# Performance work log

Measured on AMD Instinct MI355X. Metric: run time of the kernel, lower is better.

## Reference

```python
import jax, jax.numpy as jnp
import numpy as np

D_MODEL = 512
D_INNER = 1024      # expand * d_model
NHEADS = 16         # d_inner // headdim, headdim = d_model // num_heads = 64
HEADDIM = 64
DSTATE = 64
DCONV = 4           # window_size
DFF = 2048
B, LM, LT = 16, 1024, 512


def _rmsnorm(x, eps=1e-6):
    return x * jax.lax.rsqrt(jnp.mean(x * x, axis=-1, keepdims=True) + eps)


def setup_inputs():
    key = jax.random.key(0)
    ks = jax.random.split(key, 10)
    conv_dim = D_INNER + 2 * DSTATE
    d_in_proj = 2 * D_INNER + 2 * DSTATE + NHEADS
    return {
        'tgt': jax.random.normal(ks[0], (B, LT, D_MODEL), jnp.float32),
        'memory': jax.random.normal(ks[1], (B, LM, D_MODEL), jnp.float32),
        'mem_mask': jnp.ones((B, LM), jnp.float32),
        'tgt_mask': jnp.ones((B, LT), jnp.float32),
        'in_proj_w': jax.random.normal(ks[2], (d_in_proj, D_MODEL), jnp.float32) * 0.02,
        'conv_w': jax.random.normal(ks[3], (conv_dim, DCONV), jnp.float32) * 0.2,
        'conv_b': jnp.zeros((conv_dim,), jnp.float32),
        'dt_bias': jax.random.uniform(ks[4], (NHEADS,), jnp.float32, -4.0, -2.0),
        'A_log': jnp.log(jax.random.uniform(ks[5], (NHEADS,), jnp.float32, 1.0, 16.0)),
        'D': jnp.ones((NHEADS,), jnp.float32),
        'norm_w': jnp.ones((D_INNER,), jnp.float32),
        'out_proj_w': jax.random.normal(ks[6], (D_MODEL, D_INNER), jnp.float32) * 0.02,
        'fc1_w': jax.random.normal(ks[7], (DFF, D_MODEL), jnp.float32) * 0.02,
        'fc1_b': jnp.zeros((DFF,), jnp.float32),
        'fc2_w': jax.random.normal(ks[8], (D_MODEL, DFF), jnp.float32) * 0.02,
        'fc2_b': jnp.zeros((D_MODEL,), jnp.float32),
    }


def _mamba2(u, in_proj_w, conv_w, conv_b, dt_bias, A_log, D, norm_w, out_proj_w):
    # u: (B, L, d_model) -- Mamba2-style selective scan (causal, ngroups=1)
    b, L, _ = u.shape
    zxbcdt = jnp.einsum('bld,ed->ble', u, in_proj_w)  # (B,L,2192)
    z = zxbcdt[..., :D_INNER]
    xBC = zxbcdt[..., D_INNER:D_INNER + D_INNER + 2 * DSTATE]
    dt = zxbcdt[..., -NHEADS:]

    # causal depthwise conv1d, kernel = DCONV, then swish
    xBC_pad = jnp.pad(xBC, ((0, 0), (DCONV - 1, 0), (0, 0)))
    conv = conv_b
    conv = sum(conv_w[:, k] * xBC_pad[:, k:k + L] for k in range(DCONV)) + conv_b
    xBC = jax.nn.silu(conv)

    x = xBC[..., :D_INNER].reshape(b, L, NHEADS, HEADDIM)   # (B,L,H,P)
    Bm = xBC[..., D_INNER:D_INNER + DSTATE]                  # (B,L,N)
    Cm = xBC[..., D_INNER + DSTATE:]                         # (B,L,N)

    dt = jax.nn.softplus(dt + dt_bias)                       # (B,L,H)
    A = -jnp.exp(A_log)                                      # (H,)
    a = jnp.exp(dt * A)                                      # (B,L,H) decay

    def step(h, inputs):
        a_t, dt_t, x_t, B_t, C_t = inputs
        # h: (B,H,P,N)
        h = a_t[:, :, None, None] * h + (dt_t[:, :, None] * x_t)[..., None] * B_t[:, None, None, :]
        y = jnp.einsum('bhpn,bn->bhp', h, C_t)
        return h, y

    h0 = jnp.zeros((b, NHEADS, HEADDIM, DSTATE), u.dtype)
    xs = (jnp.moveaxis(a, 1, 0), jnp.moveaxis(dt, 1, 0), jnp.moveaxis(x, 1, 0),
          jnp.moveaxis(Bm, 1, 0), jnp.moveaxis(Cm, 1, 0))
    _, ys = jax.lax.scan(step, h0, xs)                       # (L,B,H,P)
    y = jnp.moveaxis(ys, 0, 1) + D[None, None, :, None] * x  # skip term
    y = y.reshape(b, L, D_INNER)

    # gated RMSNorm + out_proj
    y = y * jax.nn.silu(z)
    y = _rmsnorm(y, 1e-5) * norm_w
    return jnp.einsum('ble,de->bld', y, out_proj_w)


def _forward(tgt, memory, mem_mask, tgt_mask, in_proj_w, conv_w, conv_b, dt_bias,
             A_log, D, norm_w, out_proj_w, fc1_w, fc1_b, fc2_w, fc2_b):
    tgt = tgt * tgt_mask[..., None]
    tgt1 = _rmsnorm(tgt)
    memory = memory * mem_mask[..., None]
    u = jnp.concatenate([memory, tgt1], axis=1)
    mask = jnp.concatenate([mem_mask, tgt_mask], axis=1)
    u = u * mask[..., None]
    tgt2 = _mamba2(u, in_proj_w, conv_w, conv_b, dt_bias, A_log, D, norm_w, out_proj_w)
    tgt2 = tgt2[:, -tgt1.shape[1]:]
    tgt = tgt + tgt2  # dropout = identity (eval)
    tgt1 = _rmsnorm(tgt)
    h = jax.nn.gelu(jnp.einsum('bld,fd->blf', tgt1, fc1_w) + fc1_b, approximate=False)
    tgt2 = jnp.einsum('blf,df->bld', h, fc2_w) + fc2_b
    return tgt + tgt2


def reference(tgt, memory, mem_mask, tgt_mask, in_proj_w, conv_w, conv_b, dt_bias,
              A_log, D, norm_w, out_proj_w, fc1_w, fc1_b, fc2_w, fc2_b):
    return _forward(tgt, memory, mem_mask, tgt_mask, in_proj_w, conv_w, conv_b, dt_bias,
                    A_log, D, norm_w, out_proj_w, fc1_w, fc1_b, fc2_w, fc2_b)
```

## Files before the change

### kernel.cpp

```cpp
#include <hip/hip_runtime.h>
#include <cstddef>

#define BB 16
#define LMM 1024
#define LTT 512
#define LL 1536
#define DMODEL 512
#define DINNER 1024
#define NH 16
#define DIPROJ 2192
#define DFF2 2048

typedef __bf16 bf16_t;
typedef bf16_t bf16x2 __attribute__((ext_vector_type(2)));
typedef bf16_t bf16x4 __attribute__((ext_vector_type(4)));
typedef bf16_t bf16x8 __attribute__((ext_vector_type(8)));
typedef float f32x4 __attribute__((ext_vector_type(4)));

typedef __attribute__((address_space(3))) void lds_void;
typedef const __attribute__((address_space(1))) void glb_void;

__device__ __forceinline__ void gload16(const void* g, void* l) {
  __builtin_amdgcn_global_load_lds((glb_void*)g, (lds_void*)l, 16, 0, 0);
}

__device__ inline float block_sum(float v, float* sbuf) {
#pragma unroll
  for (int off = 32; off > 0; off >>= 1) v += __shfl_xor(v, off, 64);
  int w = threadIdx.x >> 6;
  if ((threadIdx.x & 63) == 0) sbuf[w] = v;
  __syncthreads();
  return sbuf[0] + sbuf[1] + sbuf[2] + sbuf[3];
}

__global__ __launch_bounds__(256)
void cvt_all(const float* __restrict__ s0, const float* __restrict__ s1,
             const float* __restrict__ s2, const float* __restrict__ s3,
             bf16_t* __restrict__ dst)
{
  int i = (blockIdx.x * 256 + threadIdx.x) * 4;
  if (i >= 3743744) return;
  const float* src;
  int off;
  if (i < 1122304)      { src = s0; off = i; }
  else if (i < 1646592) { src = s1; off = i - 1122304; }
  else if (i < 2695168) { src = s2; off = i - 1646592; }
  else                  { src = s3; off = i - 2695168; }
  float4 v = *(const float4*)&src[off];
  bf16x4 o;
  o[0] = (bf16_t)v.x; o[1] = (bf16_t)v.y; o[2] = (bf16_t)v.z; o[3] = (bf16_t)v.w;
  *(bf16x4*)&dst[i] = o;
}

__global__ __launch_bounds__(256)
void prep_u(const float* __restrict__ tgt, const float* __restrict__ memory,
            const float* __restrict__ mem_mask, const float* __restrict__ tgt_mask,
            bf16_t* __restrict__ u, float* __restrict__ tgtm)
{
  __shared__ float sbuf[4];
  const int row = blockIdx.x;
  const int b = row / LL;
  const int t = row - b * LL;
  const int tid = threadIdx.x;
  if (t < LMM) {
    float m = mem_mask[b * LMM + t];
    float s = m * m;
    const float* src = memory + ((size_t)b * LMM + t) * DMODEL;
    float2 v = *(const float2*)&src[tid * 2];
    bf16x2 o; o[0] = (bf16_t)(v.x * s); o[1] = (bf16_t)(v.y * s);
    *(bf16x2*)&u[(size_t)row * DMODEL + tid * 2] = o;
  } else {
    const int tt = t - LMM;
    float mk = tgt_mask[b * LTT + tt];
    const float* src = tgt + ((size_t)b * LTT + tt) * DMODEL;
    float2 v = *(const float2*)&src[tid * 2];
    v.x *= mk; v.y *= mk;
    *(float2*)&tgtm[((size_t)b * LTT + tt) * DMODEL + tid * 2] = v;
    float ss = block_sum(v.x * v.x + v.y * v.y, sbuf);
    float inv = rsqrtf(ss * (1.0f / 512.0f) + 1e-6f) * mk;
    bf16x2 o; o[0] = (bf16_t)(v.x * inv); o[1] = (bf16_t)(v.y * inv);
    *(bf16x2*)&u[(size_t)row * DMODEL + tid * 2] = o;
  }
}

template<int EPI>
__global__ __launch_bounds__(256)
void gemm_abf(const bf16_t* __restrict__ A, const bf16_t* __restrict__ W,
              int M, int N, int K,
              float* __restrict__ Cf, const float* __restrict__ bias,
              const float* __restrict__ res)
{
  const int nbx = gridDim.x;
  const int nwg = nbx * gridDim.y;
  int flat = blockIdx.y * nbx + blockIdx.x;
  int swz = (flat & 7) * (nwg >> 3) + (flat >> 3);
  const int m0 = (swz / nbx) * 128;
  const int n0 = (swz % nbx) * 128;
  __shared__ __align__(16) bf16_t As[128 * 64];
  __shared__ __align__(16) bf16_t Bs[128 * 64];
  const int tid = threadIdx.x;
  const int lane = tid & 63;
  const int wid = tid >> 6;
  const int wr = (wid >> 1) * 64, wc = (wid & 1) * 64;
  const int r = lane & 15;
  const int g = lane >> 4;
  const int r7 = r & 7;
  const int lrow = lane >> 3;
  const int sslot = (lane & 7) ^ lrow;

  int arow[4], brow[4];
#pragma unroll
  for (int ci = 0; ci < 4; ++ci) {
    int tr = wid * 32 + ci * 8 + lrow;
    arow[ci] = m0 + tr;
    int bn = n0 + tr;
    brow[ci] = bn < N ? bn : N - 1;
  }

  f32x4 acc[4][4];
#pragma unroll
  for (int m = 0; m < 4; ++m)
#pragma unroll
    for (int n = 0; n < 4; ++n) acc[m][n] = (f32x4){0.f, 0.f, 0.f, 0.f};

  for (int kt = 0; kt < K; kt += 64) {
#pragma unroll
    for (int ci = 0; ci < 4; ++ci) {
      int chunk = wid * 4 + ci;
      gload16(A + (size_t)arow[ci] * K + kt + sslot * 8, &As[chunk * 512]);
      gload16(W + (size_t)brow[ci] * K + kt + sslot * 8, &Bs[chunk * 512]);
    }
    __syncthreads();
#pragma unroll
    for (int c = 0; c < 2; ++c) {
      bf16x8 af[4], bfr[4];
#pragma unroll
      for (int m = 0; m < 4; ++m) {
        int row = wr + m * 16 + r;
        af[m] = *(const bf16x8*)&As[row * 64 + (((c * 4 + g) ^ r7) * 8)];
      }
#pragma unroll
      for (int n = 0; n < 4; ++n) {
        int row = wc + n * 16 + r;
        bfr[n] = *(const bf16x8*)&Bs[row * 64 + (((c * 4 + g) ^ r7) * 8)];
      }
#pragma unroll
      for (int m = 0; m < 4; ++m)
#pragma unroll
        for (int n = 0; n < 4; ++n)
          acc[m][n] = __builtin_amdgcn_mfma_f32_16x16x32_bf16(af[m], bfr[n], acc[m][n], 0, 0, 0);
    }
    __syncthreads();
  }

#pragma unroll
  for (int m = 0; m < 4; ++m) {
#pragma unroll
    for (int n = 0; n < 4; ++n) {
      int gcol = n0 + wc + n * 16 + r;
      if (gcol >= N) continue;
#pragma unroll
      for (int j = 0; j < 4; ++j) {
        float v = acc[m][n][j];
        int grow = m0 + wr + m * 16 + g * 4 + j;
        if (EPI == 2) v += bias[gcol] + res[(size_t)grow * N + gcol];
        else          v += res[(size_t)grow * N + gcol];
        Cf[(size_t)grow * N + gcol] = v;
      }
    }
  }
}

template<int EPI>
__global__ __launch_bounds__(512)
void gemm_big(const bf16_t* __restrict__ A, const bf16_t* __restrict__ W,
              int M, int N, int K,
              bf16_t* __restrict__ Cb, const float* __restrict__ bias,
              bf16_t* __restrict__ zbuf, bf16_t* __restrict__ xbc,
              float* __restrict__ dts, float* __restrict__ labuf,
              const float* __restrict__ dt_bias, const float* __restrict__ A_log)
{
  const int nbx = gridDim.x;
  const int nwg = nbx * gridDim.y;
  int flat = blockIdx.y * nbx + blockIdx.x;
  int swz = (flat & 7) * (nwg >> 3) + (flat >> 3);
  const int m0 = (swz / nbx) * 256;
  const int n0 = (swz % nbx) * 128;
  int bq = 0, tbase = 0;
  if (EPI == 4) {
    bq = m0 / LL; tbase = m0 - bq * LL;
    if (n0 + 128 <= DINNER && tbase + 256 <= LMM) return;
  }
  __shared__ __align__(16) bf16_t As[256 * 64];
  __shared__ __align__(16) bf16_t Bs[128 * 64];
  const int tid = threadIdx.x;
  const int lane = tid & 63;
  const int wid = tid >> 6;
  const int wr = (wid >> 1) * 64;
  const int wc = (wid & 1) * 64;
  const int r = lane & 15;
  const int g = lane >> 4;
  const int r7 = r & 7;
  const int lrow = lane >> 3;
  const int sslot = (lane & 7) ^ lrow;

  int arow[4], brow[2];
#pragma unroll
  for (int ci = 0; ci < 4; ++ci) arow[ci] = m0 + wid * 32 + ci * 8 + lrow;
#pragma unroll
  for (int ci = 0; ci < 2; ++ci) {
    int bn = n0 + wid * 16 + ci * 8 + lrow;
    brow[ci] = bn < N ? bn : N - 1;
  }

  f32x4 acc[4][4];
#pragma unroll
  for (int m = 0; m < 4; ++m)
#pragma unroll
    for (int n = 0; n < 4; ++n) acc[m][n] = (f32x4){0.f, 0.f, 0.f, 0.f};

  for (int kt = 0; kt < K; kt += 64) {
#pragma unroll
    for (int ci = 0; ci < 4; ++ci)
      gload16(A + (size_t)arow[ci] * K + kt + sslot * 8, &As[(wid * 4 + ci) * 512]);
#pragma unroll
    for (int ci = 0; ci < 2; ++ci)
      gload16(W + (size_t)brow[ci] * K + kt + sslot * 8, &Bs[(wid * 2 + ci) * 512]);
    __syncthreads();
#pragma unroll
    for (int c = 0; c < 2; ++c) {
      bf16x8 af[4], bfr[4];
#pragma unroll
      for (int m = 0; m < 4; ++m) {
        int row = wr + m * 16 + r;
        af[m] = *(const bf16x8*)&As[row * 64 + (((c * 4 + g) ^ r7) * 8)];
      }
#pragma unroll
      for (int n = 0; n < 4; ++n) {
        int row = wc + n * 16 + r;
        bfr[n] = *(const bf16x8*)&Bs[row * 64 + (((c * 4 + g) ^ r7) * 8)];
      }
#pragma unroll
      for (int m = 0; m < 4; ++m)
#pragma unroll
        for (int n = 0; n < 4; ++n)
          acc[m][n] = __builtin_amdgcn_mfma_f32_16x16x32_bf16(af[m], bfr[n], acc[m][n], 0, 0, 0);
    }
    __syncthreads();
  }

#pragma unroll
  for (int m = 0; m < 4; ++m) {
#pragma unroll
    for (int n = 0; n < 4; ++n) {
      int gcol = n0 + wc + n * 16 + r;
      if (gcol >= N) continue;
#pragma unroll
      for (int j = 0; j < 4; ++j) {
        float v = acc[m][n][j];
        int lrow2 = wr + m * 16 + g * 4 + j;
        if (EPI == 4) {
          int t = tbase + lrow2;
          if (gcol < DINNER) {
            if (t >= LMM)
              zbuf[(((size_t)(bq * LTT + t - LMM)) << 10) + gcol] = (bf16_t)v;
          } else if (gcol < DINNER + 1152) {
            xbc[(size_t)(bq * LL + t) * 1152 + (gcol - DINNER)] = (bf16_t)v;
          } else {
            int h = gcol - 2176;
            float raw = v + dt_bias[h];
            float d = raw > 20.f ? raw : log1pf(expf(raw));
            size_t ix = (size_t)(bq * LL + t) * 16 + h;
            dts[ix] = d;
            labuf[ix] = -expf(A_log[h]) * d;
          }
        } else {
          int grow = m0 + lrow2;
          v += bias[gcol];
          v = 0.5f * v * (1.f + erff(v * 0.70710678f));
          Cb[(size_t)grow * N + gcol] = (bf16_t)v;
        }
      }
    }
  }
}

__global__ __launch_bounds__(256)
void sbc_k(const bf16_t* __restrict__ xbc, const float* __restrict__ cw,
           const float* __restrict__ cb, bf16_t* __restrict__ BtG,
           bf16_t* __restrict__ Sg, bf16_t* __restrict__ CcG)
{
  __shared__ __align__(16) bf16_t rawBC[132 * 128];
  __shared__ __align__(16) bf16_t CB[128 * 128];
  __shared__ float wls[128 * 4];
  __shared__ float bls[128];
  const int c = blockIdx.x, b = blockIdx.y;
  const int t0 = c * 128;
  const int tid = threadIdx.x, lane = tid & 63, wid = tid >> 6;
  const int r = lane & 15, g = lane >> 4;

  if (tid < 128) {
    int gch = 1024 + tid;
#pragma unroll
    for (int k = 0; k < 4; ++k) wls[tid * 4 + k] = cw[gch * 4 + k];
    bls[tid] = cb[gch];
  }
#pragma unroll
  for (int ci = 0; ci < 9; ++ci) {
    int chunk = ci * 4 + wid;
    if (chunk < 33) {
      int F = chunk * 1024 + lane * 16;
      int row = F >> 8, off = F & 255;
      gload16(xbc + (size_t)(b * LL + t0 - 3 + row) * 1152 + 1024 + off / 2,
              &rawBC[chunk * 512]);
    }
  }
  __syncthreads();
  if (c == 0 && tid < 48) {
    bf16x8 z;
#pragma unroll
    for (int j = 0; j < 8; ++j) z[j] = (bf16_t)0.f;
    *(bf16x8*)&rawBC[tid * 8] = z;
  }
  __syncthreads();
#pragma unroll 2
  for (int it = 0; it < 64; ++it) {
    int o = tid + it * 256;
    int t = o >> 7, ch = o & 127;
    float a0 = bls[ch];
#pragma unroll
    for (int kk = 0; kk < 4; ++kk)
      a0 = fmaf(wls[ch * 4 + kk], (float)rawBC[(t + kk) * 128 + ch], a0);
    float sv = a0 / (1.f + expf(-a0));
    int slot = ch >> 3;
    int swslot = (slot & 8) | ((slot & 7) ^ (t & 7));
    CB[t * 128 + swslot * 8 + (ch & 7)] = (bf16_t)sv;
    if (c >= 8 && ch >= 64) {
      int n = ch - 64;
      CcG[(((size_t)(b * 4 + (c - 8)) * 128 + t)) * 64 + (((n >> 3) ^ (t & 7)) << 3) + (n & 7)] = (bf16_t)sv;
    }
  }
  __syncthreads();
  {
    int n = tid & 63, tb = tid >> 6;
#pragma unroll
    for (int s8 = 0; s8 < 4; ++s8) {
      int ts = tb * 32 + s8 * 8;
      bf16x8 v;
#pragma unroll
      for (int e = 0; e < 8; ++e) {
        int t = ts + e;
        int slot = (n >> 3) ^ (t & 7);
        v[e] = CB[t * 128 + slot * 8 + (n & 7)];
      }
      *(bf16x8*)&BtG[((size_t)(b * 12 + c) * 64 + n) * 128 + ((((ts >> 3) ^ (n & 7))) << 3)] = v;
    }
  }
  if (c >= 8) {
    f32x4 sacc[2][8];
#pragma unroll
    for (int tt = 0; tt < 2; ++tt)
#pragma unroll
      for (int ct = 0; ct < 8; ++ct) sacc[tt][ct] = (f32x4){0.f, 0.f, 0.f, 0.f};
    const int ctn = 2 * wid + 2;
#pragma unroll
    for (int kk = 0; kk < 2; ++kk) {
      bf16x8 ca[2];
#pragma unroll
      for (int tt = 0; tt < 2; ++tt) {
        int trow = wid * 32 + tt * 16 + r;
        int slot = (64 + kk * 32 + g * 8) >> 3;
        int sw = (slot & 8) | ((slot & 7) ^ (trow & 7));
        ca[tt] = *(const bf16x8*)&CB[trow * 128 + sw * 8];
      }
#pragma unroll
      for (int ct = 0; ct < 8; ++ct) {
        if (ct < ctn) {
          int taur = ct * 16 + r;
          int sw = ((kk * 4 + g) ^ (taur & 7));
          bf16x8 bb = *(const bf16x8*)&CB[taur * 128 + sw * 8];
          sacc[0][ct] = __builtin_amdgcn_mfma_f32_16x16x32_bf16(ca[0], bb, sacc[0][ct], 0, 0, 0);
          sacc[1][ct] = __builtin_amdgcn_mfma_f32_16x16x32_bf16(ca[1], bb, sacc[1][ct], 0, 0, 0);
        }
      }
    }
    size_t sbase = (size_t)(b * 4 + (c - 8)) * 16384;
#pragma unroll
    for (int tt = 0; tt < 2; ++tt)
#pragma unroll
      for (int ct = 0; ct < 8; ++ct) {
        if (ct < ctn) {
#pragma unroll
          for (int j = 0; j < 4; ++j) {
            int ta = wid * 32 + tt * 16 + g * 4 + j;
            int tau = ct * 16 + r;
            Sg[sbase + ta * 128 + (tau ^ ((ta & 7) << 3))] = (bf16_t)sacc[tt][ct][j];
          }
        }
      }
  }
}

__global__ __launch_bounds__(256)
void ssd_hend(const bf16_t* __restrict__ xbc, const float* __restrict__ dts,
              const float* __restrict__ labuf, const float* __restrict__ cw,
              const float* __restrict__ cb, const bf16_t* __restrict__ BtG,
              bf16_t* __restrict__ hend, float* __restrict__ Lacum,
              float* __restrict__ Ak)
{
  __shared__ __align__(16) bf16_t rawX[136 * 64];
  __shared__ __align__(16) bf16_t Xt[64 * 128];
  __shared__ __align__(16) bf16_t Bt[64 * 128];
  __shared__ float wv[128];
  __shared__ float wls[64 * 4];
  __shared__ float bls[64];
  const int c = blockIdx.x;
  const int bh = blockIdx.y;
  const int b = bh >> 4, h = bh & 15;
  const int t0 = c * 128;
  const int tid = threadIdx.x, lane = tid & 63, wid = tid >> 6;
  const int r = lane & 15, g = lane >> 4;

  if (tid < 64) {
    int gch = h * 64 + tid;
#pragma unroll
    for (int k = 0; k < 4; ++k) wls[tid * 4 + k] = cw[gch * 4 + k];
    bls[tid] = cb[gch];
  }
#pragma unroll
  for (int ci = 0; ci < 5; ++ci) {
    int chunk = ci * 4 + wid;
    if (chunk < 17) {
      int F = chunk * 1024 + lane * 16;
      int row = F >> 7, off = F & 127;
      gload16(xbc + (size_t)(b * LL + t0 - 3 + row) * 1152 + h * 64 + off / 2,
              &rawX[chunk * 512]);
    }
  }
#pragma unroll
  for (int ci = 0; ci < 4; ++ci) {
    int chunk = ci * 4 + wid;
    int F = chunk * 1024 + lane * 16;
    gload16(BtG + (size_t)(b * 12 + c) * 8192 + F / 2, &Bt[chunk * 512]);
  }
  __syncthreads();
  if (c == 0 && tid < 24) {
    bf16x8 z;
#pragma unroll
    for (int j = 0; j < 8; ++j) z[j] = (bf16_t)0.f;
    *(bf16x8*)&rawX[tid * 8] = z;
  }
  if (tid < 64) {
    float v0 = labuf[(size_t)(b * LL + t0 + tid) * 16 + h];
    float v1 = labuf[(size_t)(b * LL + t0 + 64 + tid) * 16 + h];
    float d0 = dts[(size_t)(b * LL + t0 + tid) * 16 + h];
    float d1 = dts[(size_t)(b * LL + t0 + 64 + tid) * 16 + h];
#pragma unroll
    for (int d = 1; d < 64; d <<= 1) { float t_ = __shfl(v0, tid - d, 64); if (tid >= d) v0 += t_; }
    float T0 = __shfl(v0, 63, 64);
#pragma unroll
    for (int d = 1; d < 64; d <<= 1) { float t_ = __shfl(v1, tid - d, 64); if (tid >= d) v1 += t_; }
    v1 += T0;
    float Ls = __shfl(v1, 63, 64);
    wv[tid] = expf(Ls - v0) * d0; wv[64 + tid] = expf(Ls - v1) * d1;
    Lacum[(size_t)(bh * 12 + c) * 128 + tid] = v0;
    Lacum[(size_t)(bh * 12 + c) * 128 + 64 + tid] = v1;
    if (tid == 0) Ak[bh * 12 + c] = expf(Ls);
  }
  __syncthreads();
  {
    int p = tid & 63, tb = (tid >> 6) * 32;
    float w0 = wls[p * 4], w1 = wls[p * 4 + 1], w2 = wls[p * 4 + 2], w3 = wls[p * 4 + 3];
    float bb0 = bls[p];
    int sw = (p & 7) << 3;
#pragma unroll
    for (int i8 = 0; i8 < 4; ++i8) {
      bf16x8 ov;
#pragma unroll
      for (int e = 0; e < 8; ++e) {
        int t = tb + i8 * 8 + e;
        float a0 = bb0;
        a0 = fmaf(w0, (float)rawX[(t + 0) * 64 + p], a0);
        a0 = fmaf(w1, (float)rawX[(t + 1) * 64 + p], a0);
        a0 = fmaf(w2, (float)rawX[(t + 2) * 64 + p], a0);
        a0 = fmaf(w3, (float)rawX[(t + 3) * 64 + p], a0);
        ov[e] = (bf16_t)(a0 / (1.f + expf(-a0)));
      }
      *(bf16x8*)&Xt[p * 128 + ((tb + i8 * 8) ^ sw)] = ov;
    }
  }
  __syncthreads();
  f32x4 acc[4];
#pragma unroll
  for (int n = 0; n < 4; ++n) acc[n] = (f32x4){0.f, 0.f, 0.f, 0.f};
  const int prow = wid * 16 + r;
#pragma unroll
  for (int kk = 0; kk < 4; ++kk) {
    int k0 = kk * 32 + g * 8;
    bf16x8 xv = *(const bf16x8*)&Xt[prow * 128 + (k0 ^ ((prow & 7) << 3))];
    bf16x8 af;
#pragma unroll
    for (int j = 0; j < 8; ++j) af[j] = (bf16_t)((float)xv[j] * wv[k0 + j]);
#pragma unroll
    for (int nt = 0; nt < 4; ++nt) {
      int nrow = nt * 16 + r;
      bf16x8 bf_ = *(const bf16x8*)&Bt[nrow * 128 + (k0 ^ ((nrow & 7) << 3))];
      acc[nt] = __builtin_amdgcn_mfma_f32_16x16x32_bf16(af, bf_, acc[nt], 0, 0, 0);
    }
  }
  size_t base = ((size_t)(bh * 12 + c)) * 4096;
#pragma unroll
  for (int nt = 0; nt < 4; ++nt)
#pragma unroll
    for (int j = 0; j < 4; ++j)
      hend[base + (size_t)(wid * 16 + g * 4 + j) * 64 + nt * 16 + r] = (bf16_t)acc[nt][j];
}

__global__ __launch_bounds__(256)
void ssd_y(const bf16_t* __restrict__ xbc, const float* __restrict__ dts,
           const bf16_t* __restrict__ hend, const float* __restrict__ Ak,
           const float* __restrict__ Lacum, const bf16_t* __restrict__ Sg,
           const bf16_t* __restrict__ CcG, const float* __restrict__ cw,
           const float* __restrict__ cb, const float* __restrict__ Dp,
           bf16_t* __restrict__ ybuf)
{
  __shared__ __align__(16) char region0[32768];
  __shared__ __align__(16) bf16_t Xt[64 * 128];
  __shared__ __align__(16) bf16_t Cs[128 * 64];
  __shared__ __align__(16) bf16_t hts[64 * 64];
  __shared__ float Lat[128];
  __shared__ float dtv[128];
  __shared__ float wls[64 * 4];
  __shared__ float bls[64];
  bf16_t* rawX = (bf16_t*)region0;
  bf16_t* Gs   = (bf16_t*)region0;
  const int c = 8 + blockIdx.x;
  const int bh = blockIdx.y;
  const int b = bh >> 4, h = bh & 15;
  const int t0 = c * 128;
  const int tid = threadIdx.x, lane = tid & 63, wid = tid >> 6;
  const int r = lane & 15, g = lane >> 4;

  if (tid < 64) {
    int gch = h * 64 + tid;
#pragma unroll
    for (int k = 0; k < 4; ++k) wls[tid * 4 + k] = cw[gch * 4 + k];
    bls[tid] = cb[gch];
  }
  if (tid < 128) {
    Lat[tid] = Lacum[(size_t)(bh * 12 + c) * 128 + tid];
    dtv[tid] = dts[(size_t)(b * LL + t0 + tid) * 16 + h];
  }
#pragma unroll
  for (int ci = 0; ci < 5; ++ci) {
    int chunk = ci * 4 + wid;
    if (chunk < 17) {
      int F = chunk * 1024 + lane * 16;
      int row = F >> 7, off = F & 127;
      gload16(xbc + (size_t)(b * LL + t0 - 3 + row) * 1152 + h * 64 + off / 2,
              &rawX[chunk * 512]);
    }
  }
#pragma unroll
  for (int ci = 0; ci < 4; ++ci) {
    int chunk = ci * 4 + wid;
    int F = chunk * 1024 + lane * 16;
    gload16(CcG + (size_t)(b * 4 + (c - 8)) * 8192 + F / 2, &Cs[chunk * 512]);
  }
  {
    float hin[16];
#pragma unroll
    for (int e = 0; e < 16; ++e) hin[e] = 0.f;
    float accp = 1.f;
    for (int k = c - 1; k >= 0; --k) {
      const bf16_t* hp = hend + ((size_t)(bh * 12 + k)) * 4096 + tid * 16;
      bf16x8 e0 = *(const bf16x8*)hp;
      bf16x8 e1 = *(const bf16x8*)(hp + 8);
#pragma unroll
      for (int j = 0; j < 8; ++j) {
        hin[j]     = fmaf(accp, (float)e0[j], hin[j]);
        hin[j + 8] = fmaf(accp, (float)e1[j], hin[j + 8]);
      }
      accp *= Ak[bh * 12 + k];
    }
    int p = tid >> 2, n0 = (tid & 3) * 16;
    bf16x8 o0, o1;
#pragma unroll
    for (int j = 0; j < 8; ++j) { o0[j] = (bf16_t)hin[j]; o1[j] = (bf16_t)hin[j + 8]; }
    int p7 = p & 7;
    *(bf16x8*)&hts[p * 64 + (((n0 >> 3) ^ p7) << 3)] = o0;
    *(bf16x8*)&hts[p * 64 + ((((n0 >> 3) + 1) ^ p7) << 3)] = o1;
  }
  __syncthreads();
  {
    int p = tid & 63, tb = (tid >> 6) * 32;
    float w0 = wls[p * 4], w1 = wls[p * 4 + 1], w2 = wls[p * 4 + 2], w3 = wls[p * 4 + 3];
    float bb0 = bls[p];
    int sw = (p & 7) << 3;
#pragma unroll
    for (int i8 = 0; i8 < 4; ++i8) {
      bf16x8 ov;
#pragma unroll
      for (int e = 0; e < 8; ++e) {
        int t = tb + i8 * 8 + e;
        float a0 = bb0;
        a0 = fmaf(w0, (float)rawX[(t + 0) * 64 + p], a0);
        a0 = fmaf(w1, (float)rawX[(t + 1) * 64 + p], a0);
        a0 = fmaf(w2, (float)rawX[(t + 2) * 64 + p], a0);
        a0 = fmaf(w3, (float)rawX[(t + 3) * 64 + p], a0);
        ov[e] = (bf16_t)(a0 / (1.f + expf(-a0)));
      }
      *(bf16x8*)&Xt[p * 128 + ((tb + i8 * 8) ^ sw)] = ov;
    }
  }
  __syncthreads();
  {
    size_t sbase = (size_t)(b * 4 + (c - 8)) * 16384;
#pragma unroll
    for (int it = 0; it < 8; ++it) {
      int o = tid + it * 256;
      int ta = o >> 4, sl = o & 15;
      bf16x8 sv = *(const bf16x8*)&Sg[sbase + ta * 128 + sl * 8];
      int tau0 = (sl ^ (ta & 7)) * 8;
      float Lta = Lat[ta];
      bf16x8 gv;
#pragma unroll
      for (int e = 0; e < 8; ++e) {
        int tau = tau0 + e;
        float xa = (tau <= ta) ? (Lta - Lat[tau]) : -1e30f;
        gv[e] = (bf16_t)(expf(xa) * dtv[tau] * (float)sv[e]);
      }
      *(bf16x8*)&Gs[ta * 128 + sl * 8] = gv;
    }
  }
  __syncthreads();

  bf16x8 caf[2][2];
#pragma unroll
  for (int tt = 0; tt < 2; ++tt)
#pragma unroll
    for (int kk = 0; kk < 2; ++kk) {
      int trow = wid * 32 + tt * 16 + r;
      caf[tt][kk] = *(const bf16x8*)&Cs[trow * 64 + ((((kk * 4 + g)) ^ (trow & 7)) << 3)];
    }

  f32x4 accY[2][4], acc2[2][4];
#pragma unroll
  for (int tt = 0; tt < 2; ++tt)
#pragma unroll
    for (int pt = 0; pt < 4; ++pt) {
      accY[tt][pt] = (f32x4){0.f, 0.f, 0.f, 0.f};
      acc2[tt][pt] = (f32x4){0.f, 0.f, 0.f, 0.f};
    }
#pragma unroll
  for (int tt = 0; tt < 2; ++tt) {
    int trow = wid * 32 + tt * 16 + r;
#pragma unroll
    for (int kk = 0; kk < 4; ++kk) {
      if (kk <= wid) {
        int k0 = kk * 32 + g * 8;
        bf16x8 ga = *(const bf16x8*)&Gs[trow * 128 + (k0 ^ ((trow & 7) << 3))];
#pragma unroll
        for (int pt = 0; pt < 4; ++pt) {
          int prow = pt * 16 + r;
          bf16x8 xb = *(const bf16x8*)&Xt[prow * 128 + (k0 ^ ((prow & 7) << 3))];
          accY[tt][pt] = __builtin_amdgcn_mfma_f32_16x16x32_bf16(ga, xb, accY[tt][pt], 0, 0, 0);
        }
      }
    }
#pragma unroll
    for (int kk = 0; kk < 2; ++kk) {
#pragma unroll
      for (int pt = 0; pt < 4; ++pt) {
        int prow = pt * 16 + r;
        bf16x8 hb = *(const bf16x8*)&hts[prow * 64 + ((((kk * 4 + g)) ^ (prow & 7)) << 3)];
        acc2[tt][pt] = __builtin_amdgcn_mfma_f32_16x16x32_bf16(caf[tt][kk], hb, acc2[tt][pt], 0, 0, 0);
      }
    }
  }

  const float Dh = Dp[h];
#pragma unroll
  for (int tt = 0; tt < 2; ++tt) {
#pragma unroll
    for (int j = 0; j < 4; ++j) {
      int trow = wid * 32 + tt * 16 + g * 4 + j;
      float el = expf(Lat[trow]);
      size_t yrow = ((size_t)(b * LTT + (c - 8) * 128 + trow)) << 10;
#pragma unroll
      for (int pt = 0; pt < 4; ++pt) {
        int p = pt * 16 + r;
        float xv = (float)Xt[p * 128 + (trow ^ ((p & 7) << 3))];
        float yv = accY[tt][pt][j] + el * acc2[tt][pt][j] + Dh * xv;
        ybuf[yrow + h * 64 + p] = (bf16_t)yv;
      }
    }
  }
}

__global__ __launch_bounds__(256)
void gate_norm_k(const bf16_t* __restrict__ zbuf, const bf16_t* __restrict__ ybuf,
                 const float* __restrict__ norm_w, bf16_t* __restrict__ yn)
{
  __shared__ float sbuf[4];
  const int row = blockIdx.x;
  const int tid = threadIdx.x;
  bf16x4 yv = *(const bf16x4*)&ybuf[(size_t)row * DINNER + tid * 4];
  bf16x4 zv = *(const bf16x4*)&zbuf[(size_t)row * DINNER + tid * 4];
  float v[4];
#pragma unroll
  for (int c = 0; c < 4; ++c) {
    float y = (float)yv[c], z = (float)zv[c];
    v[c] = y * (z / (1.f + expf(-z)));
  }
  float ss = block_sum(v[0]*v[0] + v[1]*v[1] + v[2]*v[2] + v[3]*v[3], sbuf);
  float inv = rsqrtf(ss * (1.f / 1024.f) + 1e-5f);
  float4 nw = *(const float4*)&norm_w[tid * 4];
  bf16x4 o;
  o[0] = (bf16_t)(v[0] * inv * nw.x); o[1] = (bf16_t)(v[1] * inv * nw.y);
  o[2] = (bf16_t)(v[2] * inv * nw.z); o[3] = (bf16_t)(v[3] * inv * nw.w);
  *(bf16x4*)&yn[(size_t)row * DINNER + tid * 4] = o;
}

__global__ __launch_bounds__(256)
void rms_k(const float* __restrict__ in, bf16_t* __restrict__ out)
{
  __shared__ float sbuf[4];
  const int row = blockIdx.x;
  const int tid = threadIdx.x;
  float2 v = *(const float2*)&in[(size_t)row * DMODEL + tid * 2];
  float ss = block_sum(v.x * v.x + v.y * v.y, sbuf);
  float inv = rsqrtf(ss * (1.f / 512.f) + 1e-6f);
  bf16x2 o; o[0] = (bf16_t)(v.x * inv); o[1] = (bf16_t)(v.y * inv);
  *(bf16x2*)&out[(size_t)row * DMODEL + tid * 2] = o;
}

extern "C" void kernel_launch(void* const* d_in, const int* in_sizes, int n_in,
                              void* d_out, int out_size, void* d_ws, size_t ws_size,
                              hipStream_t stream)
{
  const float* tgt        = (const float*)d_in[0];
  const float* memory     = (const float*)d_in[1];
  const float* mem_mask   = (const float*)d_in[2];
  const float* tgt_mask   = (const float*)d_in[3];
  const float* in_proj_w  = (const float*)d_in[4];
  const float* conv_w     = (const float*)d_in[5];
  const float* conv_b     = (const float*)d_in[6];
  const float* dt_bias    = (const float*)d_in[7];
  const float* A_log      = (const float*)d_in[8];
  const float* Dp         = (const float*)d_in[9];
  const float* norm_w     = (const float*)d_in[10];
  const float* out_proj_w = (const float*)d_in[11];
  const float* fc1_w      = (const float*)d_in[12];
  const float* fc1_b      = (const float*)d_in[13];
  const float* fc2_w      = (const float*)d_in[14];
  const float* fc2_b      = (const float*)d_in[15];

  char* wsb = (char*)d_ws;
  bf16_t* u     = (bf16_t*)(wsb + 0);
  bf16_t* zbuf  = (bf16_t*)(wsb + 25165824);
  bf16_t* xbc   = (bf16_t*)(wsb + 41943040);
  float*  dts   = (float*)(wsb + 98566144);
  float*  labuf = (float*)(wsb + 100139008);
  float*  tgtm  = (float*)(wsb + 101711872);
  bf16_t* hend  = (bf16_t*)(wsb + 118489088);
  float*  Lacum = (float*)(wsb + 143667200);
  float*  Akb   = (float*)(wsb + 145240064);
  bf16_t* BtG   = (bf16_t*)(wsb + 145252352);
  bf16_t* Sg    = (bf16_t*)(wsb + 148398080);
  bf16_t* CcG   = (bf16_t*)(wsb + 150495232);
  bf16_t* wip   = (bf16_t*)(wsb + 160444416);
  bf16_t* wop   = wip + 1122304;
  bf16_t* wf1   = wop + 524288;
  bf16_t* wf2   = wf1 + 1048576;
  bf16_t* ybuf  = (bf16_t*)(wsb + 0);
  bf16_t* yn    = (bf16_t*)(wsb + 41943040);
  float*  tres  = (float*)(wsb + 58720256);
  bf16_t* t1    = (bf16_t*)(wsb + 75497472);
  bf16_t* hbuf  = (bf16_t*)(wsb + 0);
  float* outp = (float*)d_out;

  cvt_all<<<3656, 256, 0, stream>>>(in_proj_w, out_proj_w, fc1_w, fc2_w, wip);
  prep_u<<<BB * LL, 256, 0, stream>>>(tgt, memory, mem_mask, tgt_mask, u, tgtm);
  gemm_big<4><<<dim3(18, 96), 512, 0, stream>>>(u, wip, BB * LL, DIPROJ, DMODEL,
      nullptr, nullptr, zbuf, xbc, dts, labuf, dt_bias, A_log);
  sbc_k<<<dim3(12, BB), 256, 0, stream>>>(xbc, conv_w, conv_b, BtG, Sg, CcG);
  ssd_hend<<<dim3(12, BB * NH), 256, 0, stream>>>(xbc, dts, labuf, conv_w, conv_b,
      BtG, hend, Lacum, Akb);
  ssd_y<<<dim3(4, BB * NH), 256, 0, stream>>>(xbc, dts, hend, Akb, Lacum, Sg, CcG,
      conv_w, conv_b, Dp, ybuf);
  gate_norm_k<<<BB * LTT, 256, 0, stream>>>(zbuf, ybuf, norm_w, yn);
  gemm_abf<3><<<dim3(4, 64), 256, 0, stream>>>(yn, wop, BB * LTT, DMODEL, DINNER,
      tres, nullptr, tgtm);
  rms_k<<<BB * LTT, 256, 0, stream>>>(tres, t1);
  gemm_big<1><<<dim3(16, 32), 512, 0, stream>>>(t1, wf1, BB * LTT, DFF2, DMODEL,
      hbuf, fc1_b, nullptr, nullptr, nullptr, nullptr, nullptr, nullptr);
  gemm_abf<2><<<dim3(4, 64), 256, 0, stream>>>(hbuf, wf2, BB * LTT, DMODEL, DFF2,
      outp, fc2_b, tres);
}
```

Baseline: 301.5 us.

## Double-buffer LDS in GEMM kernels with BK=32 and prefetch next tile

Both bf16 GEMM kernels switch from a single 64-wide K tile with two barriers per iteration to two 32-wide K tile buffers. The next tile's global-to-LDS loads are issued before the MFMAs on the current tile, and there is one barrier per iteration. The LDS swizzle changes to match the 32-element row width. The aim is to hide global load latency behind compute. In exchange there are twice as many loop iterations with less MFMA work per barrier.

```diff
diff --git a/kernel.cpp b/kernel.cpp
--- a/kernel.cpp
+++ b/kernel.cpp
@@ -96,60 +96,65 @@
   int swz = (flat & 7) * (nwg >> 3) + (flat >> 3);
   const int m0 = (swz / nbx) * 128;
   const int n0 = (swz % nbx) * 128;
-  __shared__ __align__(16) bf16_t As[128 * 64];
-  __shared__ __align__(16) bf16_t Bs[128 * 64];
+  __shared__ __align__(16) bf16_t As[2][128 * 32];
+  __shared__ __align__(16) bf16_t Bs[2][128 * 32];
   const int tid = threadIdx.x;
   const int lane = tid & 63;
   const int wid = tid >> 6;
   const int wr = (wid >> 1) * 64, wc = (wid & 1) * 64;
   const int r = lane & 15;
   const int g = lane >> 4;
-  const int r7 = r & 7;
-  const int lrow = lane >> 3;
-  const int sslot = (lane & 7) ^ lrow;
-
-  int arow[4], brow[4];
-#pragma unroll
-  for (int ci = 0; ci < 4; ++ci) {
-    int tr = wid * 32 + ci * 8 + lrow;
+  const int rk = (r >> 1) & 3;
+  const int lrow4 = lane >> 2;
+  const int sslot = (lane & 3) ^ ((lrow4 >> 1) & 3);
+
+  int arow[2], brow[2];
+#pragma unroll
+  for (int ci = 0; ci < 2; ++ci) {
+    int tr = wid * 32 + ci * 16 + lrow4;
     arow[ci] = m0 + tr;
     int bn = n0 + tr;
     brow[ci] = bn < N ? bn : N - 1;
   }
 
+  auto stage = [&](int buf, int kt) {
+#pragma unroll
+    for (int ci = 0; ci < 2; ++ci) {
+      int chunk = wid * 2 + ci;
+      gload16(A + (size_t)arow[ci] * K + kt + sslot * 8, &As[buf][chunk * 512]);
+      gload16(W + (size_t)brow[ci] * K + kt + sslot * 8, &Bs[buf][chunk * 512]);
+    }
+  };
+
   f32x4 acc[4][4];
 #pragma unroll
   for (int m = 0; m < 4; ++m)
 #pragma unroll
     for (int n = 0; n < 4; ++n) acc[m][n] = (f32x4){0.f, 0.f, 0.f, 0.f};
 
-  for (int kt = 0; kt < K; kt += 64) {
-#pragma unroll
-    for (int ci = 0; ci < 4; ++ci) {
-      int chunk = wid * 4 + ci;
-      gload16(A + (size_t)arow[ci] * K + kt + sslot * 8, &As[chunk * 512]);
-      gload16(W + (size_t)brow[ci] * K + kt + sslot * 8, &Bs[chunk * 512]);
-    }
-    __syncthreads();
-#pragma unroll
-    for (int c = 0; c < 2; ++c) {
-      bf16x8 af[4], bfr[4];
-#pragma unroll
-      for (int m = 0; m < 4; ++m) {
-        int row = wr + m * 16 + r;
-        af[m] = *(const bf16x8*)&As[row * 64 + (((c * 4 + g) ^ r7) * 8)];
-      }
-#pragma unroll
-      for (int n = 0; n < 4; ++n) {
-        int row = wc + n * 16 + r;
-        bfr[n] = *(const bf16x8*)&Bs[row * 64 + (((c * 4 + g) ^ r7) * 8)];
-      }
-#pragma unroll
-      for (int m = 0; m < 4; ++m)
-#pragma unroll
-        for (int n = 0; n < 4; ++n)
-          acc[m][n] = __builtin_amdgcn_mfma_f32_16x16x32_bf16(af[m], bfr[n], acc[m][n], 0, 0, 0);
-    }
+  const int NK = K >> 5;
+  stage(0, 0);
+  __syncthreads();
+  for (int ki = 0; ki < NK; ++ki) {
+    const int cur = ki & 1;
+    if (ki + 1 < NK) stage(cur ^ 1, (ki + 1) << 5);
+    bf16x8 af[4], bfr[4];
+    const int sl = (g ^ rk) * 8;
+#pragma unroll
+    for (int m = 0; m < 4; ++m) {
+      int row = wr + m * 16 + r;
+      af[m] = *(const bf16x8*)&As[cur][row * 32 + sl];
+    }
+#pragma unroll
+    for (int n = 0; n < 4; ++n) {
+      int row = wc + n * 16 + r;
+      bfr[n] = *(const bf16x8*)&Bs[cur][row * 32 + sl];
+    }
+#pragma unroll
+    for (int m = 0; m < 4; ++m)
+#pragma unroll
+      for (int n = 0; n < 4; ++n)
+        acc[m][n] = __builtin_amdgcn_mfma_f32_16x16x32_bf16(af[m], bfr[n], acc[m][n], 0, 0, 0);
     __syncthreads();
   }
 
@@ -191,8 +196,8 @@
     bq = m0 / LL; tbase = m0 - bq * LL;
     if (n0 + 128 <= DINNER && tbase + 256 <= LMM) return;
   }
-  __shared__ __align__(16) bf16_t As[256 * 64];
-  __shared__ __align__(16) bf16_t Bs[128 * 64];
+  __shared__ __align__(16) bf16_t As[2][256 * 32];
+  __shared__ __align__(16) bf16_t Bs[2][128 * 32];
   const int tid = threadIdx.x;
   const int lane = tid & 63;
   const int wid = tid >> 6;
@@ -200,18 +205,24 @@
   const int wc = (wid & 1) * 64;
   const int r = lane & 15;
   const int g = lane >> 4;
-  const int r7 = r & 7;
-  const int lrow = lane >> 3;
-  const int sslot = (lane & 7) ^ lrow;
-
-  int arow[4], brow[2];
-#pragma unroll
-  for (int ci = 0; ci < 4; ++ci) arow[ci] = m0 + wid * 32 + ci * 8 + lrow;
-#pragma unroll
-  for (int ci = 0; ci < 2; ++ci) {
-    int bn = n0 + wid * 16 + ci * 8 + lrow;
-    brow[ci] = bn < N ? bn : N - 1;
-  }
+  const int rk = (r >> 1) & 3;
+  const int lrow4 = lane >> 2;
+  const int sslot = (lane & 3) ^ ((lrow4 >> 1) & 3);
+
+  int arow[2], brow;
+#pragma unroll
+  for (int ci = 0; ci < 2; ++ci) arow[ci] = m0 + wid * 32 + ci * 16 + lrow4;
+  {
+    int bn = n0 + wid * 16 + lrow4;
+    brow = bn < N ? bn : N - 1;
+  }
+
+  auto stage = [&](int buf, int kt) {
+#pragma unroll
+    for (int ci = 0; ci < 2; ++ci)
+      gload16(A + (size_t)arow[ci] * K + kt + sslot * 8, &As[buf][(wid * 2 + ci) * 512]);
+    gload16(W + (size_t)brow * K + kt + sslot * 8, &Bs[buf][wid * 512]);
+  };
 
   f32x4 acc[4][4];
 #pragma unroll
@@ -219,33 +230,29 @@
 #pragma unroll
     for (int n = 0; n < 4; ++n) acc[m][n] = (f32x4){0.f, 0.f, 0.f, 0.f};
 
-  for (int kt = 0; kt < K; kt += 64) {
-#pragma unroll
-    for (int ci = 0; ci < 4; ++ci)
-      gload16(A + (size_t)arow[ci] * K + kt + sslot * 8, &As[(wid * 4 + ci) * 512]);
-#pragma unroll
-    for (int ci = 0; ci < 2; ++ci)
-      gload16(W + (size_t)brow[ci] * K + kt + sslot * 8, &Bs[(wid * 2 + ci) * 512]);
-    __syncthreads();
-#pragma unroll
-    for (int c = 0; c < 2; ++c) {
-      bf16x8 af[4], bfr[4];
-#pragma unroll
-      for (int m = 0; m < 4; ++m) {
-        int row = wr + m * 16 + r;
-        af[m] = *(const bf16x8*)&As[row * 64 + (((c * 4 + g) ^ r7) * 8)];
-      }
-#pragma unroll
-      for (int n = 0; n < 4; ++n) {
-        int row = wc + n * 16 + r;
-        bfr[n] = *(const bf16x8*)&Bs[row * 64 + (((c * 4 + g) ^ r7) * 8)];
-      }
-#pragma unroll
-      for (int m = 0; m < 4; ++m)
-#pragma unroll
-        for (int n = 0; n < 4; ++n)
-          acc[m][n] = __builtin_amdgcn_mfma_f32_16x16x32_bf16(af[m], bfr[n], acc[m][n], 0, 0, 0);
-    }
+  const int NK = K >> 5;
+  stage(0, 0);
+  __syncthreads();
+  for (int ki = 0; ki < NK; ++ki) {
+    const int cur = ki & 1;
+    if (ki + 1 < NK) stage(cur ^ 1, (ki + 1) << 5);
+    bf16x8 af[4], bfr[4];
+    const int sl = (g ^ rk) * 8;
+#pragma unroll
+    for (int m = 0; m < 4; ++m) {
+      int row = wr + m * 16 + r;
+      af[m] = *(const bf16x8*)&As[cur][row * 32 + sl];
+    }
+#pragma unroll
+    for (int n = 0; n < 4; ++n) {
+      int row = wc + n * 16 + r;
+      bfr[n] = *(const bf16x8*)&Bs[cur][row * 32 + sl];
+    }
+#pragma unroll
+    for (int m = 0; m < 4; ++m)
+#pragma unroll
+      for (int n = 0; n < 4; ++n)
+        acc[m][n] = __builtin_amdgcn_mfma_f32_16x16x32_bf16(af[m], bfr[n], acc[m][n], 0, 0, 0);
     __syncthreads();
   }
 
```

Result: slower. 309.2 us (+2.6%).
